# Kernel optimization log

Hardware: AMD Instinct MI355X
Metric: run time of the kernel (lower is better)

The kernel has to match this reference:

```python
import jax, jax.numpy as jnp
import numpy as np

H = 16         # num query heads
KV = 8         # num kv heads
HD = 64        # head_dim
WINDOW = 512   # sliding window size
ROPE_BASE = 10000.0


def rotate_half(x):
    x1, x2 = x[..., : x.shape[-1] // 2], x[..., x.shape[-1] // 2 :]
    return jnp.concatenate((-x2, x1), axis=-1)


def rope_cos_sin(seq_len, dim, dtype):
    inv_freq = 1.0 / (ROPE_BASE ** (jnp.arange(0, dim, 2, dtype=jnp.float32) / dim))
    t = jnp.arange(seq_len, dtype=jnp.float32)
    freqs = jnp.outer(t, inv_freq)              # [S, dim/2]
    emb = jnp.concatenate((freqs, freqs), axis=-1)  # [S, dim]
    return jnp.cos(emb).astype(dtype), jnp.sin(emb).astype(dtype)


def setup_inputs() -> dict:
    key = jax.random.key(0)
    ks = jax.random.split(key, 5)
    B, S, D = 2, 2048, 1024
    std = 0.02
    return {
        "hidden_states": jax.random.normal(ks[0], (B, S, D), dtype=jnp.float32),
        "Wq": jax.random.normal(ks[1], (D, H * HD), dtype=jnp.float32) * std,
        "Wk": jax.random.normal(ks[2], (D, KV * HD), dtype=jnp.float32) * std,
        "Wv": jax.random.normal(ks[3], (D, KV * HD), dtype=jnp.float32) * std,
        "Wo": jax.random.normal(ks[4], (H * HD, D), dtype=jnp.float32) * std,
    }


def reference(hidden_states, Wq, Wk, Wv, Wo):
    B, S, D = hidden_states.shape
    n_rep = H // KV

    q = (hidden_states @ Wq).reshape(B, S, H, HD).transpose(0, 2, 1, 3)   # [B,H,S,hd]
    k = (hidden_states @ Wk).reshape(B, S, KV, HD).transpose(0, 2, 1, 3)  # [B,KV,S,hd]
    v = (hidden_states @ Wv).reshape(B, S, KV, HD).transpose(0, 2, 1, 3)

    cos, sin = rope_cos_sin(S, HD, q.dtype)  # [S,hd]
    cos = cos[None, None]
    sin = sin[None, None]
    q = q * cos + rotate_half(q) * sin
    k = k * cos + rotate_half(k) * sin

    # repeat kv heads for GQA ([:, :, None] expand + reshape == repeat along head axis)
    k = jnp.repeat(k, n_rep, axis=1)  # [B,H,S,hd]
    v = jnp.repeat(v, n_rep, axis=1)

    scores = jnp.einsum("bhqd,bhkd->bhqk", q, k) / jnp.sqrt(jnp.asarray(HD, q.dtype))
    i = jnp.arange(S)[:, None]
    j = jnp.arange(S)[None, :]
    allowed = (j <= i) & (j >= i - WINDOW)  # causal + sliding window
    scores = jnp.where(allowed[None, None], scores, -jnp.inf)

    attn = jax.nn.softmax(scores, axis=-1)
    out = jnp.einsum("bhqk,bhkd->bhqd", attn, v)          # [B,H,S,hd]
    out = out.transpose(0, 2, 1, 3).reshape(B, S, H * HD)  # [B,S,D]
    return out @ Wo
```

## Files before the change

### kernel.cpp

```cpp
#include <hip/hip_runtime.h>
#include <hip/hip_bf16.h>

typedef __attribute__((ext_vector_type(8))) short short8;
typedef __attribute__((ext_vector_type(4))) float f32x4;

#define S_LEN 2048
#define NH 16
#define NKV 8
#define HD 64
#define WIN 512
#define DMODEL 1024
#define LOG2_10000 13.287712379549449f

#define GLOAD16(g, l)                                                        \
    __builtin_amdgcn_global_load_lds(                                        \
        (const __attribute__((address_space(1))) unsigned int*)(g),          \
        (__attribute__((address_space(3))) unsigned int*)(l), 16, 0, 0)

__global__ void prep_kernel(const float* __restrict__ X,
                            const float* __restrict__ W0,
                            const float* __restrict__ W1,
                            const float* __restrict__ W2,
                            const float* __restrict__ W3,
                            __hip_bfloat16* __restrict__ Xb,
                            __hip_bfloat16* __restrict__ WqkvT,
                            __hip_bfloat16* __restrict__ WoT) {
    if (blockIdx.z == 4) {
        int tid = (blockIdx.y * 32 + blockIdx.x) * 256 + threadIdx.y * 32 + threadIdx.x;
        const float4* Xi = reinterpret_cast<const float4*>(X);
#pragma unroll
        for (int r = 0; r < 4; ++r) {
            int i = tid + r * (1024 * 256);
            float4 v = Xi[i];
            alignas(8) __hip_bfloat16 h[4];
            h[0] = __float2bfloat16(v.x);
            h[1] = __float2bfloat16(v.y);
            h[2] = __float2bfloat16(v.z);
            h[3] = __float2bfloat16(v.w);
            *reinterpret_cast<ushort4*>(Xb + (size_t)i * 4) =
                *reinterpret_cast<ushort4*>(h);
        }
        return;
    }
    __shared__ float tile[32][33];
    const int K = DMODEL;
    const float* W;
    __hip_bfloat16* WT;
    int N;
    switch (blockIdx.z) {
        case 0: W = W0; WT = WqkvT;                          N = 1024; break;
        case 1: W = W1; WT = WqkvT + (size_t)1024 * K;       N = 512;  break;
        case 2: W = W2; WT = WqkvT + (size_t)1536 * K;       N = 512;  break;
        default: W = W3; WT = WoT;                           N = 1024; break;
    }
    if ((int)blockIdx.x * 32 >= N) return;
    int nx = blockIdx.x * 32 + threadIdx.x;
    int k0 = blockIdx.y * 32;
#pragma unroll
    for (int r = 0; r < 4; ++r) {
        int k = k0 + threadIdx.y + r * 8;
        tile[threadIdx.y + r * 8][threadIdx.x] = W[(size_t)k * N + nx];
    }
    __syncthreads();
#pragma unroll
    for (int r = 0; r < 4; ++r) {
        int nn = blockIdx.x * 32 + threadIdx.y + r * 8;
        int kk = k0 + threadIdx.x;
        WT[(size_t)nn * K + kk] = __float2bfloat16(tile[threadIdx.x][threadIdx.y + r * 8]);
    }
}

__global__ __launch_bounds__(256, 2) void gemm_qkv_kernel(
    const __hip_bfloat16* __restrict__ A,
    const __hip_bfloat16* __restrict__ BT,
    __hip_bfloat16* __restrict__ Qo,
    __hip_bfloat16* __restrict__ Ko,
    __hip_bfloat16* __restrict__ VTo) {
    const int K = DMODEL;
    __shared__ __hip_bfloat16 ldsA[2][128 * 64];
    __shared__ __hip_bfloat16 ldsB[2][128 * 64];
    const int tx = threadIdx.x;
    const int wave = tx >> 6;
    const int lane = tx & 63;
    const int l16 = lane & 15;
    const int quad = lane >> 4;
    const int col0 = blockIdx.x * 128;
    const int row0 = blockIdx.y * 128;
    const int wrow = (wave >> 1) * 64;
    const int wcol = (wave & 1) * 64;
    const int sw = l16 & 7;

    f32x4 acc[4][4] = {};

    const int arow = tx >> 3;
    const int cs8 = ((tx & 7) ^ (arow & 7)) * 8;
    const __hip_bfloat16* gA = A + (size_t)(row0 + arow) * K + cs8;
    const __hip_bfloat16* gB = BT + (size_t)(col0 + arow) * K + cs8;

    auto stage = [&](int k0, int bf) {
        char* lA = (char*)(&ldsA[bf][0]) + tx * 16;
        char* lB = (char*)(&ldsB[bf][0]) + tx * 16;
#pragma unroll
        for (int r = 0; r < 4; ++r) {
            GLOAD16(gA + (size_t)(r * 32) * K + k0, lA + r * 4096);
            GLOAD16(gB + (size_t)(r * 32) * K + k0, lB + r * 4096);
        }
    };

    stage(0, 0);
    int buf = 0;
    for (int k0 = 0; k0 < K; k0 += 64) {
        __syncthreads();
        if (k0 + 64 < K) stage(k0 + 64, buf ^ 1);
        short8 af[4][2], bf4[4][2];
#pragma unroll
        for (int i = 0; i < 4; ++i) {
            const char* ar = (const char*)(&ldsA[buf][0]) + (wrow + i * 16 + l16) * 128;
            const char* br = (const char*)(&ldsB[buf][0]) + (wcol + i * 16 + l16) * 128;
#pragma unroll
            for (int ks = 0; ks < 2; ++ks) {
                af[i][ks] = *reinterpret_cast<const short8*>(
                    ar + (((ks * 4 + quad) ^ sw) << 4));
                bf4[i][ks] = *reinterpret_cast<const short8*>(
                    br + (((ks * 4 + quad) ^ sw) << 4));
            }
        }
#pragma unroll
        for (int ks = 0; ks < 2; ++ks)
#pragma unroll
            for (int mi = 0; mi < 4; ++mi)
#pragma unroll
                for (int ni = 0; ni < 4; ++ni)
                    acc[mi][ni] = __builtin_amdgcn_mfma_f32_16x16x32_bf16(
                        af[mi][ks], bf4[ni][ks], acc[mi][ni], 0, 0, 0);
        buf ^= 1;
    }

    const int rbase = row0 + wrow;
    const int cbaseg = col0 + wcol;
    const bool isQ = (cbaseg < DMODEL);
    const bool isK = (cbaseg >= DMODEL) && (cbaseg < DMODEL + 512);
    if (isQ || isK) {
        float invf[2];
        invf[0] = exp2f(-(float)(l16)      * (LOG2_10000 / 32.0f));
        invf[1] = exp2f(-(float)(16 + l16) * (LOG2_10000 / 32.0f));
#pragma unroll
        for (int mi = 0; mi < 4; ++mi)
#pragma unroll
            for (int r = 0; r < 4; ++r) {
                int srow = (rbase + mi * 16 + quad * 4 + r) & (S_LEN - 1);
#pragma unroll
                for (int ni = 0; ni < 2; ++ni) {
                    float ang = (float)srow * invf[ni];
                    float c = __cosf(ang), s = __sinf(ang);
                    float x1 = acc[mi][ni][r], x2 = acc[mi][ni + 2][r];
                    acc[mi][ni][r]     = x1 * c - x2 * s;
                    acc[mi][ni + 2][r] = x2 * c + x1 * s;
                }
            }
        __hip_bfloat16* Co = isQ ? Qo : Ko;
        int cbase = isQ ? cbaseg : cbaseg - DMODEL;
        int rowstride = isQ ? (NH * HD) : (NKV * HD);
#pragma unroll
        for (int mi = 0; mi < 4; ++mi)
#pragma unroll
            for (int ni = 0; ni < 4; ++ni) {
                size_t col = cbase + ni * 16 + l16;
#pragma unroll
                for (int r = 0; r < 4; ++r)
                    Co[(size_t)(rbase + mi * 16 + quad * 4 + r) * rowstride + col] =
                        __float2bfloat16(acc[mi][ni][r]);
            }
    } else {
        int bb = row0 >> 11;
#pragma unroll
        for (int mi = 0; mi < 4; ++mi) {
            int s = ((rbase + mi * 16 + quad * 4) & (S_LEN - 1));
#pragma unroll
            for (int ni = 0; ni < 4; ++ni) {
                int colv = cbaseg - 1536 + ni * 16 + l16;
                int vh = colv >> 6, d = colv & 63;
                alignas(8) __hip_bfloat16 hv[4];
#pragma unroll
                for (int r = 0; r < 4; ++r) hv[r] = __float2bfloat16(acc[mi][ni][r]);
                *reinterpret_cast<ushort4*>(
                    VTo + ((size_t)(bb * NKV + vh) * HD + d) * S_LEN + s) =
                    *reinterpret_cast<ushort4*>(hv);
            }
        }
    }
}

__global__ __launch_bounds__(128, 2) void gemm_op_kernel(
    const __hip_bfloat16* __restrict__ A,
    const __hip_bfloat16* __restrict__ BT,
    float* __restrict__ Co, int N, int K) {
    __shared__ __hip_bfloat16 ldsA[2][128 * 64];
    __shared__ __hip_bfloat16 ldsB[2][64 * 64];
    const int tx = threadIdx.x;
    const int wave = tx >> 6;
    const int lane = tx & 63;
    const int l16 = lane & 15;
    const int quad = lane >> 4;
    const int col0 = blockIdx.x * 64;
    const int row0 = blockIdx.y * 128;
    const int wrow = wave * 64;
    const int sw = l16 & 7;

    f32x4 acc[4][4] = {};

    const int arow = tx >> 3;
    const int cs8 = ((tx & 7) ^ (arow & 7)) * 8;
    const __hip_bfloat16* gA = A + (size_t)(row0 + arow) * K + cs8;
    const __hip_bfloat16* gB = BT + (size_t)(col0 + arow) * K + cs8;

    auto stage = [&](int k0, int bf) {
        char* lA = (char*)(&ldsA[bf][0]) + tx * 16;
        char* lB = (char*)(&ldsB[bf][0]) + tx * 16;
#pragma unroll
        for (int r = 0; r < 8; ++r)
            GLOAD16(gA + (size_t)(r * 16) * K + k0, lA + r * 2048);
#pragma unroll
        for (int r = 0; r < 4; ++r)
            GLOAD16(gB + (size_t)(r * 16) * K + k0, lB + r * 2048);
    };

    stage(0, 0);
    int buf = 0;
    for (int k0 = 0; k0 < K; k0 += 64) {
        __syncthreads();
        if (k0 + 64 < K) stage(k0 + 64, buf ^ 1);
        short8 af[4][2], bf4[4][2];
#pragma unroll
        for (int i = 0; i < 4; ++i) {
            const char* ar = (const char*)(&ldsA[buf][0]) + (wrow + i * 16 + l16) * 128;
            const char* br = (const char*)(&ldsB[buf][0]) + (i * 16 + l16) * 128;
#pragma unroll
            for (int ks = 0; ks < 2; ++ks) {
                af[i][ks] = *reinterpret_cast<const short8*>(
                    ar + (((ks * 4 + quad) ^ sw) << 4));
                bf4[i][ks] = *reinterpret_cast<const short8*>(
                    br + (((ks * 4 + quad) ^ sw) << 4));
            }
        }
#pragma unroll
        for (int ks = 0; ks < 2; ++ks)
#pragma unroll
            for (int mi = 0; mi < 4; ++mi)
#pragma unroll
                for (int ni = 0; ni < 4; ++ni)
                    acc[mi][ni] = __builtin_amdgcn_mfma_f32_16x16x32_bf16(
                        af[mi][ks], bf4[ni][ks], acc[mi][ni], 0, 0, 0);
        buf ^= 1;
    }

    const int rbase = row0 + wrow;
#pragma unroll
    for (int mi = 0; mi < 4; ++mi)
#pragma unroll
        for (int ni = 0; ni < 4; ++ni) {
            size_t col = col0 + ni * 16 + l16;
#pragma unroll
            for (int r = 0; r < 4; ++r)
                Co[(size_t)(rbase + mi * 16 + quad * 4 + r) * N + col] = acc[mi][ni][r];
        }
}

__global__ __launch_bounds__(256, 4) void attn_mfma_kernel(
    const __hip_bfloat16* __restrict__ Q,
    const __hip_bfloat16* __restrict__ K,
    const __hip_bfloat16* __restrict__ VT,
    __hip_bfloat16* __restrict__ O) {
    __shared__ __hip_bfloat16 ldsK[2][64][64];
    __shared__ __hip_bfloat16 ldsVT[2][64][64];
    __shared__ __hip_bfloat16 ldsP[4][16][64];
    const int tx = threadIdx.x;
    const int wave = tx >> 6;
    const int lane = tx & 63;
    const int l16 = lane & 15;
    const int quad = lane >> 4;
    const int q0 = blockIdx.x * 64;
    const int h = blockIdx.y;
    const int kvh = h >> 1;
    const int b = blockIdx.z;
    const int qi = q0 + wave * 16 + l16;

    short8 aq[2];
    {
        const __hip_bfloat16* qp =
            Q + (size_t)(b * S_LEN + qi) * (NH * HD) + h * HD + quad * 8;
        aq[0] = *reinterpret_cast<const short8*>(qp);
        aq[1] = *reinterpret_cast<const short8*>(qp + 32);
    }
    f32x4 acc_o[4] = {};
    float m = -1e30f, l = 0.f;
    const float SL2 = 0.125f * 1.4426950408889634f;

    const int s_row = tx >> 3;
    const int s_c8 = (((tx & 7) ^ (s_row & 7))) * 8;
    const int sw = (l16 & 7);
    auto stage = [&](int j0, int bf) {
        char* lk = (char*)(&ldsK[bf][0][0]) + tx * 16;
        char* lv = (char*)(&ldsVT[bf][0][0]) + tx * 16;
#pragma unroll
        for (int r = 0; r < 2; ++r) {
            int row = s_row + r * 32;
            GLOAD16(K + (size_t)(b * S_LEN + j0 + row) * (NKV * HD) + kvh * HD + s_c8,
                    lk + r * 4096);
            GLOAD16(VT + ((size_t)(b * NKV + kvh) * HD + row) * S_LEN + j0 + s_c8,
                    lv + r * 4096);
        }
    };

    const int kstart = (q0 >= WIN) ? (q0 - WIN) : 0;
    stage(kstart, 0);
    int buf = 0;

    char* prow = (char*)(&ldsP[wave][l16][0]);

    for (int j0 = kstart; j0 <= q0; j0 += 64) {
        __syncthreads();
        if (j0 + 64 <= q0) stage(j0 + 64, buf ^ 1);

        f32x4 sacc[4] = {};
#pragma unroll
        for (int t = 0; t < 4; ++t) {
            const __hip_bfloat16* krow = &ldsK[buf][t * 16 + l16][0];
            short8 bk0 = *reinterpret_cast<const short8*>(krow + ((quad ^ sw) * 8));
            short8 bk1 = *reinterpret_cast<const short8*>(krow + (((4 + quad) ^ sw) * 8));
            sacc[t] = __builtin_amdgcn_mfma_f32_16x16x32_bf16(bk0, aq[0], sacc[t], 0, 0, 0);
            sacc[t] = __builtin_amdgcn_mfma_f32_16x16x32_bf16(bk1, aq[1], sacc[t], 0, 0, 0);
        }

        const bool need_mask = (j0 == q0) || (q0 >= WIN && j0 == kstart);
        float sv[4][4];
        if (need_mask) {
#pragma unroll
            for (int t = 0; t < 4; ++t)
#pragma unroll
                for (int r = 0; r < 4; ++r) {
                    int j = j0 + t * 16 + quad * 4 + r;
                    bool ok = (j <= qi) && (j + WIN >= qi);
                    sv[t][r] = ok ? sacc[t][r] * SL2 : -1e30f;
                }
        } else {
#pragma unroll
            for (int t = 0; t < 4; ++t)
#pragma unroll
                for (int r = 0; r < 4; ++r) sv[t][r] = sacc[t][r] * SL2;
        }
        float cm = -1e30f;
#pragma unroll
        for (int t = 0; t < 4; ++t)
#pragma unroll
            for (int r = 0; r < 4; ++r) cm = fmaxf(cm, sv[t][r]);
        cm = fmaxf(cm, __shfl_xor(cm, 16));
        cm = fmaxf(cm, __shfl_xor(cm, 32));
        if (!__all(cm - m <= 8.0f)) {
            float mn = fmaxf(m, cm);
            float alpha = exp2f(m - mn);
            m = mn;
            l *= alpha;
#pragma unroll
            for (int t = 0; t < 4; ++t)
#pragma unroll
                for (int r = 0; r < 4; ++r) acc_o[t][r] *= alpha;
        }
        float sp = 0.f;
#pragma unroll
        for (int t = 0; t < 4; ++t)
#pragma unroll
            for (int r = 0; r < 4; ++r) { sv[t][r] = exp2f(sv[t][r] - m); sp += sv[t][r]; }
        sp += __shfl_xor(sp, 16);
        sp += __shfl_xor(sp, 32);
        l += sp;
#pragma unroll
        for (int t = 0; t < 4; ++t) {
            alignas(8) __hip_bfloat16 hp[4];
#pragma unroll
            for (int r = 0; r < 4; ++r) hp[r] = __float2bfloat16(sv[t][r]);
            int swb = ((((2 * t + (quad >> 1)) ^ (l16 & 7)) << 4) | ((quad & 1) << 3));
            *reinterpret_cast<ushort4*>(prow + swb) = *reinterpret_cast<ushort4*>(hp);
        }

#pragma unroll
        for (int ks = 0; ks < 2; ++ks) {
            short8 pf = *reinterpret_cast<const short8*>(
                prow + (((4 * ks + quad) ^ (l16 & 7)) << 4));
#pragma unroll
            for (int t = 0; t < 4; ++t) {
                const __hip_bfloat16* vrow = &ldsVT[buf][t * 16 + l16][0];
                short8 vf = *reinterpret_cast<const short8*>(
                    vrow + (((ks * 4 + quad) ^ sw) * 8));
                acc_o[t] = __builtin_amdgcn_mfma_f32_16x16x32_bf16(vf, pf, acc_o[t], 0, 0, 0);
            }
        }
        buf ^= 1;
    }

    {
        float inv = 1.f / l;
        __hip_bfloat16* op =
            O + (size_t)(b * S_LEN + qi) * (NH * HD) + h * HD;
#pragma unroll
        for (int t = 0; t < 4; ++t) {
            alignas(8) __hip_bfloat16 ho[4];
#pragma unroll
            for (int r = 0; r < 4; ++r) ho[r] = __float2bfloat16(acc_o[t][r] * inv);
            *reinterpret_cast<ushort4*>(op + t * 16 + quad * 4) =
                *reinterpret_cast<ushort4*>(ho);
        }
    }
}

extern "C" void kernel_launch(void* const* d_in, const int* in_sizes, int n_in,
                              void* d_out, int out_size, void* d_ws, size_t ws_size,
                              hipStream_t stream) {
    const float* X  = (const float*)d_in[0];
    const float* Wq = (const float*)d_in[1];
    const float* Wk = (const float*)d_in[2];
    const float* Wv = (const float*)d_in[3];
    const float* Wo = (const float*)d_in[4];
    float* out = (float*)d_out;

    const int ROWS = 2 * S_LEN;
    char* ws = (char*)d_ws;
    size_t off = 0;
    __hip_bfloat16* Xb     = (__hip_bfloat16*)(ws + off); off += (size_t)ROWS * DMODEL * 2;
    __hip_bfloat16* WqkvT  = (__hip_bfloat16*)(ws + off); off += (size_t)2048 * DMODEL * 2;
    __hip_bfloat16* WoT    = (__hip_bfloat16*)(ws + off); off += (size_t)DMODEL * DMODEL * 2;
    __hip_bfloat16* Qb     = (__hip_bfloat16*)(ws + off); off += (size_t)ROWS * (NH * HD) * 2;
    __hip_bfloat16* Kb     = (__hip_bfloat16*)(ws + off); off += (size_t)ROWS * (NKV * HD) * 2;
    __hip_bfloat16* VTg    = (__hip_bfloat16*)(ws + off); off += (size_t)ROWS * (NKV * HD) * 2;
    __hip_bfloat16* Ob     = (__hip_bfloat16*)(ws + off); off += (size_t)ROWS * (NH * HD) * 2;

    prep_kernel<<<dim3(32, 32, 5), dim3(32, 8), 0, stream>>>(
        X, Wq, Wk, Wv, Wo, Xb, WqkvT, WoT);

    gemm_qkv_kernel<<<dim3(2048 / 128, ROWS / 128), 256, 0, stream>>>(
        Xb, WqkvT, Qb, Kb, VTg);

    attn_mfma_kernel<<<dim3(S_LEN / 64, NH, 2), 256, 0, stream>>>(Qb, Kb, VTg, Ob);

    gemm_op_kernel<<<dim3(DMODEL / 64, ROWS / 128), 128, 0, stream>>>(
        Ob, WoT, out, DMODEL, DMODEL);
}
```

Before: 149.7 us.

## Split-K the output projection GEMM with 128x128 tiles and atomic accumulation

The output projection GEMM now uses 256-thread blocks computing 128x128 tiles, and splits K=1024 into two halves across blockIdx.z. Partial results are combined with float atomic adds. The output buffer is zeroed by an extra slice in the prep kernel. This doubles per-wave reuse and keeps the grid at 512 blocks, at the cost of atomic traffic and an extra zero-fill pass over the output.

Result: slower. 168.8 us (+12.8%).

```diff
diff --git a/kernel.cpp b/kernel.cpp
--- a/kernel.cpp
+++ b/kernel.cpp
@@ -24,7 +24,16 @@
                             const float* __restrict__ W3,
                             __hip_bfloat16* __restrict__ Xb,
                             __hip_bfloat16* __restrict__ WqkvT,
-                            __hip_bfloat16* __restrict__ WoT) {
+                            __hip_bfloat16* __restrict__ WoT,
+                            float* __restrict__ Oz) {
+    if (blockIdx.z == 5) {
+        int tid = (blockIdx.y * 32 + blockIdx.x) * 256 + threadIdx.y * 32 + threadIdx.x;
+        float4 z = {0.f, 0.f, 0.f, 0.f};
+        float4* Oi = reinterpret_cast<float4*>(Oz);
+#pragma unroll
+        for (int r = 0; r < 4; ++r) Oi[tid + r * (1024 * 256)] = z;
+        return;
+    }
     if (blockIdx.z == 4) {
         int tid = (blockIdx.y * 32 + blockIdx.x) * 256 + threadIdx.y * 32 + threadIdx.x;
         const float4* Xi = reinterpret_cast<const float4*>(X);
@@ -191,50 +200,51 @@
     }
 }
 
-__global__ __launch_bounds__(128, 2) void gemm_op_kernel(
+__global__ __launch_bounds__(256, 2) void gemm_op_kernel(
     const __hip_bfloat16* __restrict__ A,
     const __hip_bfloat16* __restrict__ BT,
     float* __restrict__ Co, int N, int K) {
     __shared__ __hip_bfloat16 ldsA[2][128 * 64];
-    __shared__ __hip_bfloat16 ldsB[2][64 * 64];
+    __shared__ __hip_bfloat16 ldsB[2][128 * 64];
     const int tx = threadIdx.x;
     const int wave = tx >> 6;
     const int lane = tx & 63;
     const int l16 = lane & 15;
     const int quad = lane >> 4;
-    const int col0 = blockIdx.x * 64;
+    const int col0 = blockIdx.x * 128;
     const int row0 = blockIdx.y * 128;
-    const int wrow = wave * 64;
+    const int kbase = blockIdx.z * 512;
+    const int wrow = (wave >> 1) * 64;
+    const int wcol = (wave & 1) * 64;
     const int sw = l16 & 7;
 
     f32x4 acc[4][4] = {};
 
     const int arow = tx >> 3;
     const int cs8 = ((tx & 7) ^ (arow & 7)) * 8;
-    const __hip_bfloat16* gA = A + (size_t)(row0 + arow) * K + cs8;
-    const __hip_bfloat16* gB = BT + (size_t)(col0 + arow) * K + cs8;
+    const __hip_bfloat16* gA = A + (size_t)(row0 + arow) * K + kbase + cs8;
+    const __hip_bfloat16* gB = BT + (size_t)(col0 + arow) * K + kbase + cs8;
 
     auto stage = [&](int k0, int bf) {
         char* lA = (char*)(&ldsA[bf][0]) + tx * 16;
         char* lB = (char*)(&ldsB[bf][0]) + tx * 16;
 #pragma unroll
-        for (int r = 0; r < 8; ++r)
-            GLOAD16(gA + (size_t)(r * 16) * K + k0, lA + r * 2048);
-#pragma unroll
-        for (int r = 0; r < 4; ++r)
-            GLOAD16(gB + (size_t)(r * 16) * K + k0, lB + r * 2048);
+        for (int r = 0; r < 4; ++r) {
+            GLOAD16(gA + (size_t)(r * 32) * K + k0, lA + r * 4096);
+            GLOAD16(gB + (size_t)(r * 32) * K + k0, lB + r * 4096);
+        }
     };
 
     stage(0, 0);
     int buf = 0;
-    for (int k0 = 0; k0 < K; k0 += 64) {
+    for (int k0 = 0; k0 < 512; k0 += 64) {
         __syncthreads();
-        if (k0 + 64 < K) stage(k0 + 64, buf ^ 1);
+        if (k0 + 64 < 512) stage(k0 + 64, buf ^ 1);
         short8 af[4][2], bf4[4][2];
 #pragma unroll
         for (int i = 0; i < 4; ++i) {
             const char* ar = (const char*)(&ldsA[buf][0]) + (wrow + i * 16 + l16) * 128;
-            const char* br = (const char*)(&ldsB[buf][0]) + (i * 16 + l16) * 128;
+            const char* br = (const char*)(&ldsB[buf][0]) + (wcol + i * 16 + l16) * 128;
 #pragma unroll
             for (int ks = 0; ks < 2; ++ks) {
                 af[i][ks] = *reinterpret_cast<const short8*>(
@@ -255,14 +265,17 @@
     }
 
     const int rbase = row0 + wrow;
+    const int cbase = col0 + wcol;
 #pragma unroll
     for (int mi = 0; mi < 4; ++mi)
 #pragma unroll
         for (int ni = 0; ni < 4; ++ni) {
-            size_t col = col0 + ni * 16 + l16;
+            size_t col = cbase + ni * 16 + l16;
 #pragma unroll
             for (int r = 0; r < 4; ++r)
-                Co[(size_t)(rbase + mi * 16 + quad * 4 + r) * N + col] = acc[mi][ni][r];
+                unsafeAtomicAdd(
+                    &Co[(size_t)(rbase + mi * 16 + quad * 4 + r) * N + col],
+                    acc[mi][ni][r]);
         }
 }
 
@@ -434,14 +447,14 @@
     __hip_bfloat16* VTg    = (__hip_bfloat16*)(ws + off); off += (size_t)ROWS * (NKV * HD) * 2;
     __hip_bfloat16* Ob     = (__hip_bfloat16*)(ws + off); off += (size_t)ROWS * (NH * HD) * 2;
 
-    prep_kernel<<<dim3(32, 32, 5), dim3(32, 8), 0, stream>>>(
-        X, Wq, Wk, Wv, Wo, Xb, WqkvT, WoT);
+    prep_kernel<<<dim3(32, 32, 6), dim3(32, 8), 0, stream>>>(
+        X, Wq, Wk, Wv, Wo, Xb, WqkvT, WoT, out);
 
     gemm_qkv_kernel<<<dim3(2048 / 128, ROWS / 128), 256, 0, stream>>>(
         Xb, WqkvT, Qb, Kb, VTg);
 
     attn_mfma_kernel<<<dim3(S_LEN / 64, NH, 2), 256, 0, stream>>>(Qb, Kb, VTg, Ob);
 
-    gemm_op_kernel<<<dim3(DMODEL / 64, ROWS / 128), 128, 0, stream>>>(
+    gemm_op_kernel<<<dim3(DMODEL / 128, ROWS / 128, 2), 256, 0, stream>>>(
         Ob, WoT, out, DMODEL, DMODEL);
 }
```
